# Performance work log

Hardware: AMD Instinct MI355X
Metric: run time of the kernel (lower is better)

Reference implementation:

```python
import jax, jax.numpy as jnp
import numpy as np

NEG_SLOPE = 0.01  # nn.LeakyReLU default


def conv3x3(x, w, b):
    # x: [B,C,H,W], w: [O,I,3,3], stride 1, pad 1
    y = jax.lax.conv_general_dilated(x, w, (1, 1), 'SAME',
                                     dimension_numbers=('NCHW', 'OIHW', 'NCHW'))
    return y + b[None, :, None, None]


def bilinear_gather(img, ys, xs):
    # img: [B,C,H,W]; ys, xs: [B,K,H,W] float sample coords -> [B,C,K,H,W]
    B, C, H, W = img.shape
    imgf = img.reshape(B, C, H * W)
    y0 = jnp.floor(ys)
    x0 = jnp.floor(xs)
    out = jnp.zeros((B, C) + ys.shape[1:], img.dtype)
    for dy in (0, 1):
        for dx in (0, 1):
            yc = y0 + dy
            xc = x0 + dx
            wgt = (1.0 - jnp.abs(ys - yc)) * (1.0 - jnp.abs(xs - xc))
            valid = (yc >= 0) & (yc <= H - 1) & (xc >= 0) & (xc <= W - 1)
            wgt = jnp.where(valid, wgt, 0.0)
            idx = (jnp.clip(yc, 0, H - 1) * W + jnp.clip(xc, 0, W - 1)).astype(jnp.int32)
            g = jax.vmap(lambda f, i: f[:, i])(imgf, idx)  # [B,C,K,H,W]
            out = out + wgt[:, None] * g
    return out


def dcn_v2(x, off_feat, w_off, b_off, w, b):
    # Modulated deformable 3x3 conv (DCNv2Pack, extra_offset_mask=True, dg=1).
    B, C, H, W = x.shape
    om = conv3x3(off_feat, w_off, b_off)            # [B, 27, H, W]
    o1, o2, m = jnp.split(om, 3, axis=1)            # each [B, 9, H, W]
    off = jnp.concatenate([o1, o2], axis=1)         # [B, 18, H, W]
    off_y = off[:, 0::2]                            # [B, 9, H, W]
    off_x = off[:, 1::2]
    mask = jax.nn.sigmoid(m)                        # [B, 9, H, W]
    k = jnp.arange(3, dtype=x.dtype) - 1.0
    ky = jnp.repeat(k, 3)                           # row-major kernel order
    kx = jnp.tile(k, 3)
    hh = jnp.arange(H, dtype=x.dtype)[:, None]
    ww = jnp.arange(W, dtype=x.dtype)[None, :]
    ys = hh[None, None] + ky[None, :, None, None] + off_y
    xs = ww[None, None] + kx[None, :, None, None] + off_x
    sampled = bilinear_gather(x, ys, xs)            # [B,C,9,H,W]
    wk = w.reshape(w.shape[0], C, 9)
    out = jnp.einsum('oik,bkhw,bikhw->bohw', wk, mask, sampled)
    return out + b[None, :, None, None]


def setup_inputs() -> dict:
    key = jax.random.key(0)
    ks = jax.random.split(key, 12)
    B, C, OC, H, W = 4, 64, 32, 128, 128
    s = 0.02
    return {
        'input': jax.random.normal(ks[0], (B, C, H, W), jnp.float32),
        'offset': jax.random.normal(ks[1], (B, OC, H, W), jnp.float32),
        'w_off1': jax.random.normal(ks[2], (27, OC, 3, 3), jnp.float32) * s,
        'b_off1': jnp.zeros((27,), jnp.float32),
        'w1': jax.random.normal(ks[3], (C, C, 3, 3), jnp.float32) * s,
        'b1': jnp.zeros((C,), jnp.float32),
        'w_off2': jax.random.normal(ks[4], (27, OC, 3, 3), jnp.float32) * s,
        'b_off2': jnp.zeros((27,), jnp.float32),
        'w2': jax.random.normal(ks[5], (C, C, 3, 3), jnp.float32) * s,
        'b2': jnp.zeros((C,), jnp.float32),
        'w_last': jax.random.normal(ks[6], (C, C, 3, 3), jnp.float32) * s,
        'b_last': jnp.zeros((C,), jnp.float32),
    }


def reference(input, offset, w_off1, b_off1, w1, b1,
              w_off2, b_off2, w2, b2, w_last, b_last):
    x = dcn_v2(input, offset, w_off1, b_off1, w1, b1)
    x = jnp.where(x >= 0, x, NEG_SLOPE * x)
    out = dcn_v2(x, offset, w_off2, b_off2, w2, b2) + input
    return conv3x3(out, w_last, b_last)
```

## Files before the change

### kernel.cpp

```cpp
#include <hip/hip_runtime.h>
#include <cmath>

#define HW   16384
#define Wd   128
#define Hd   128
#define NB   4

typedef __attribute__((ext_vector_type(8))) _Float16 h16x8;
typedef __attribute__((ext_vector_type(4))) float f32x4;
typedef __attribute__((ext_vector_type(4))) unsigned int u32x4;

__device__ inline unsigned short f2h(float f) {
    _Float16 h = (_Float16)f;
    return __builtin_bit_cast(unsigned short, h);
}
__device__ inline _Float16 u2h(unsigned short u) {
    return __builtin_bit_cast(_Float16, u);
}

__device__ inline void repack_one(int idx, const float* __restrict__ s1, const float* __restrict__ s2,
                                  int Osplit, int O, int CIN, int KS, unsigned short* __restrict__ dst) {
    int e    = idx & 7;
    int lane = (idx >> 3) & 63;
    int ks   = (idx >> 9) % KS;
    int m    = (idx / (512 * KS)) & 3;
    int k    = idx / (2048 * KS);
    int oc = m * 16 + (lane & 15);
    int c  = ks * 32 + (lane >> 4) * 8 + e;
    float v = 0.f;
    if (oc < O && c < CIN)
        v = (oc < Osplit) ? s1[((size_t)oc * CIN + c) * 9 + k]
                          : s2[((size_t)(oc - Osplit) * CIN + c) * 9 + k];
    dst[idx] = f2h(v);
}

__global__ __launch_bounds__(256) void prep(
    const float* __restrict__ input, const float* __restrict__ offset,
    const float* __restrict__ w_off1, const float* __restrict__ w_off2,
    const float* __restrict__ b_off1, const float* __restrict__ b_off2,
    const float* __restrict__ w1, const float* __restrict__ w2, const float* __restrict__ w_last,
    unsigned short* __restrict__ xn, unsigned short* __restrict__ offn,
    unsigned short* __restrict__ wfo, unsigned short* __restrict__ wf1,
    unsigned short* __restrict__ wf2, unsigned short* __restrict__ wfl,
    float* __restrict__ bias54)
{
    int blk = blockIdx.x;
    if (blk < 512) {
        int t = blk * 256 + threadIdx.x;
        if (t < 65536) {
            int b = t >> 14, p = t & 16383;
            const float* s = input + ((size_t)b * 64) * HW + p;
            unsigned short* d = xn + (size_t)t * 64;
#pragma unroll
            for (int g = 0; g < 8; g++) {
                unsigned short pk[8];
#pragma unroll
                for (int e = 0; e < 8; e++) pk[e] = f2h(s[(size_t)(g * 8 + e) * HW]);
                *(u32x4*)(d + g * 8) = *(u32x4*)pk;
            }
        } else {
            int u = t - 65536;
            int b = u >> 14, p = u & 16383;
            const float* s = offset + ((size_t)b * 32) * HW + p;
            unsigned short* d = offn + (size_t)u * 32;
#pragma unroll
            for (int g = 0; g < 4; g++) {
                unsigned short pk[8];
#pragma unroll
                for (int e = 0; e < 8; e++) pk[e] = f2h(s[(size_t)(g * 8 + e) * HW]);
                *(u32x4*)(d + g * 8) = *(u32x4*)pk;
            }
        }
    } else {
        int u = (blk - 512) * 256 + threadIdx.x;
        if (u < 18432)        repack_one(u, w_off1, w_off1, 27, 27, 32, 1, wfo);
        else if (u < 36864)   repack_one(u - 18432, w_off2, w_off2, 27, 27, 32, 1, wfo + 18432);
        else if (u < 73728)   repack_one(u - 36864, w1, w1, 64, 64, 64, 2, wf1);
        else if (u < 110592)  repack_one(u - 73728, w2, w2, 64, 64, 64, 2, wf2);
        else if (u < 147456)  repack_one(u - 110592, w_last, w_last, 64, 64, 64, 2, wfl);
        else if (u < 147510) {
            int j = u - 147456;
            bias54[j] = (j < 27) ? b_off1[j] : b_off2[j - 27];
        }
    }
}

__global__ __launch_bounds__(512, 8) void conv_stage64(
    const unsigned short* __restrict__ xn, const unsigned short* __restrict__ wf,
    const float* __restrict__ bias, float* __restrict__ out)
{
    __shared__ __align__(16) unsigned short stage[198 * 64];
    int lb = ((blockIdx.x & 7) << 7) | (blockIdx.x >> 3);
    int t = threadIdx.x;
    int pxbase = lb * 64;
    int b = pxbase >> 14;
    int pbase = pxbase & 16383;
    int rowbase = pbase >> 7, colbase = pbase & 127;
    const unsigned short* xb = xn + ((size_t)(b << 14)) * 64;

    for (int q = t; q < 1584; q += 512) {
        int ps = q >> 3, j = q & 7;
        int ly = ps / 66, lx = ps - ly * 66;
        int y = rowbase - 1 + ly, x = colbase - 1 + lx;
        bool ok = (y >= 0) & (y < Hd) & (x >= 0) & (x < Wd);
        u32x4 v = {0, 0, 0, 0};
        if (ok) v = *(const u32x4*)(xb + ((size_t)(y * Wd + x)) * 64 + j * 8);
        *(u32x4*)(stage + ps * 64 + ((j ^ (ps & 7)) << 3)) = v;
    }
    __syncthreads();

    int lane = t & 63;
    int wave = t >> 6;
    int kh = wave >> 2;
    int wv = wave & 3;
    int sp = wv * 16 + (lane & 15);
    int px = pxbase + sp;
    int p = px & 16383;
    int cg = lane >> 4;
    int cch = kh * 4 + cg;

    const h16x8* wfv = (const h16x8*)wf;
    f32x4 acc[4];
#pragma unroll
    for (int m = 0; m < 4; m++) acc[m] = (f32x4){0.f, 0.f, 0.f, 0.f};

#pragma unroll
    for (int k = 0; k < 9; k++) {
        int ps = (k / 3) * 66 + sp + (k % 3);
        h16x8 bq = *(const h16x8*)(stage + ps * 64 + ((cch ^ (ps & 7)) << 3));
        h16x8 aF[4];
#pragma unroll
        for (int m = 0; m < 4; m++)
            aF[m] = wfv[((k * 4 + m) * 2 + kh) * 64 + lane];
#pragma unroll
        for (int m = 0; m < 4; m++)
            acc[m] = __builtin_amdgcn_mfma_f32_16x16x32_f16(aF[m], bq, acc[m], 0, 0, 0);
    }

    __syncthreads();
    float* red = (float*)stage;
    if (kh == 1) {
#pragma unroll
        for (int m = 0; m < 4; m++)
#pragma unroll
            for (int j = 0; j < 4; j++)
                red[(m * 4 + j) * 256 + wv * 64 + lane] = acc[m][j];
    }
    __syncthreads();
    if (kh == 0) {
#pragma unroll
        for (int m = 0; m < 4; m++) {
            int ocb = m * 16 + cg * 4;
#pragma unroll
            for (int r = 0; r < 4; r++) {
                int oc = ocb + r;
                float v = acc[m][r] + red[(m * 4 + r) * 256 + wv * 64 + lane] + bias[oc];
                out[((size_t)b * 64 + oc) * HW + p] = v;
            }
        }
    }
}

struct Tap { float w00, w01, w10, w11; int o00, o01, o10, o11; };

__device__ inline Tap mkparams(float oy, float ox, float mv, int row, int col, int k) {
    Tap P;
    float mk = 1.f / (1.f + __expf(-mv));
    float ys = (float)(row + k / 3 - 1) + oy;
    float xs = (float)(col + k % 3 - 1) + ox;
    float y0f = floorf(ys), x0f = floorf(xs);
    float fy = ys - y0f, fx = xs - x0f;
    int y0 = (int)y0f, x0 = (int)x0f;
    int y1 = y0 + 1, x1 = x0 + 1;
    bool vy0 = (y0 >= 0) & (y0 < Hd);
    bool vy1 = (y1 >= 0) & (y1 < Hd);
    bool vx0 = (x0 >= 0) & (x0 < Wd);
    bool vx1 = (x1 >= 0) & (x1 < Wd);
    P.w00 = (vy0 && vx0) ? (1.f - fy) * (1.f - fx) * mk : 0.f;
    P.w01 = (vy0 && vx1) ? (1.f - fy) * fx * mk : 0.f;
    P.w10 = (vy1 && vx0) ? fy * (1.f - fx) * mk : 0.f;
    P.w11 = (vy1 && vx1) ? fy * fx * mk : 0.f;
    int iy0 = min(max(y0, 0), Hd - 1) * Wd;
    int iy1 = min(max(y1, 0), Hd - 1) * Wd;
    int ix0 = min(max(x0, 0), Wd - 1);
    int ix1 = min(max(x1, 0), Wd - 1);
    P.o00 = iy0 + ix0; P.o01 = iy0 + ix1; P.o10 = iy1 + ix0; P.o11 = iy1 + ix1;
    return P;
}

template<int EPI>
__global__ __launch_bounds__(512, 4) void dcn_fused(
    const unsigned short* __restrict__ xn, const unsigned short* __restrict__ offn,
    const unsigned short* __restrict__ wfo, const float* __restrict__ obias,
    const unsigned short* __restrict__ wf, const float* __restrict__ bias,
    const unsigned short* __restrict__ residn, unsigned short* __restrict__ outn)
{
    __shared__ __align__(16) unsigned short stage[490 * 64];
    __shared__ __align__(16) unsigned tbl[576 * 4];

    unsigned short* offstage = stage;
    float* omt = (float*)(stage + 6336);

    int lb = ((blockIdx.x & 7) << 7) | (blockIdx.x >> 3);
    int t = threadIdx.x;
    int pxbase = lb * 64;
    int b = pxbase >> 14;
    int pbase = pxbase & 16383;
    int rowbase = pbase >> 7;
    int colbase = pbase & 127;
    int ybase = rowbase - 3;
    int xbase = colbase - 3;
    const unsigned short* xb = xn + ((size_t)(b << 14)) * 64;
    const unsigned short* ob = offn + ((size_t)(b << 14)) * 32;

    for (int q = t; q < 792; q += 512) {
        int ps = q >> 2, j = q & 3;
        int ly = ps / 66, lx = ps - ly * 66;
        int y = rowbase - 1 + ly, x = colbase - 1 + lx;
        bool ok = (y >= 0) & (y < Hd) & (x >= 0) & (x < Wd);
        u32x4 v = {0, 0, 0, 0};
        if (ok) v = *(const u32x4*)(ob + ((size_t)(y * Wd + x)) * 32 + j * 8);
        *(u32x4*)(offstage + ps * 32 + ((j ^ (ps & 3)) << 3)) = v;
    }
    __syncthreads();

    int lane = t & 63;
    int wave = t >> 6;

    if (wave < 4) {
        int osp = wave * 16 + (lane & 15);
        int cg4 = lane >> 4;
        const h16x8* wfv = (const h16x8*)wfo;
        f32x4 oacc[2];
#pragma unroll
        for (int m = 0; m < 2; m++) oacc[m] = (f32x4){0.f, 0.f, 0.f, 0.f};
#pragma unroll
        for (int k = 0; k < 9; k++) {
            int ps = (k / 3) * 66 + osp + (k % 3);
            h16x8 bq = *(const h16x8*)(offstage + ps * 32 + ((cg4 ^ (ps & 3)) << 3));
#pragma unroll
            for (int m = 0; m < 2; m++) {
                h16x8 aF = wfv[(k * 4 + m) * 64 + lane];
                oacc[m] = __builtin_amdgcn_mfma_f32_16x16x32_f16(aF, bq, oacc[m], 0, 0, 0);
            }
        }
#pragma unroll
        for (int m = 0; m < 2; m++) {
            int ocb = m * 16 + cg4 * 4;
#pragma unroll
            for (int r = 0; r < 4; r++) {
                int oc = ocb + r;
                if (oc < 27) omt[oc * 64 + osp] = oacc[m][r] + obias[oc];
            }
        }
    }
    __syncthreads();

    for (int s = t; s < 576; s += 512) {
        int k = s >> 6, sp2 = s & 63;
        int row = rowbase, col = colbase + sp2;
        float oy = omt[(2 * k) * 64 + sp2];
        float ox = omt[(2 * k + 1) * 64 + sp2];
        float mv = omt[(18 + k) * 64 + sp2];
        Tap P = mkparams(oy, ox, mv, row, col, k);

        unsigned a[4];
        int oo[4] = {P.o00, P.o01, P.o10, P.o11};
#pragma unroll
        for (int c = 0; c < 4; c++) {
            int o = oo[c];
            int y = o >> 7, x = o & 127;
            int ly = y - ybase, lx = x - xbase;
            bool inw = ((unsigned)ly < 7u) & ((unsigned)lx < 70u);
            int ps = min(max(ly, 0), 6) * 70 + min(max(lx, 0), 69);
            a[c] = inw ? (unsigned)((ps << 3) | (ps & 7)) : (0x8000u | (unsigned)o);
        }
        u32x4 pk4 = { a[0] | (a[1] << 16),
                      a[2] | (a[3] << 16),
                      (unsigned)f2h(P.w00) | ((unsigned)f2h(P.w01) << 16),
                      (unsigned)f2h(P.w10) | ((unsigned)f2h(P.w11) << 16) };
        *(u32x4*)&tbl[s * 4] = pk4;
    }
    __syncthreads();

    for (int q = t; q < 3920; q += 512) {
        int ps = q >> 3, j = q & 7;
        int ly = ps / 70, lx = ps - ly * 70;
        int y = min(max(ybase + ly, 0), Hd - 1);
        int x = min(max(xbase + lx, 0), Wd - 1);
        u32x4 v = *(const u32x4*)(xb + ((size_t)(y * Wd + x)) * 64 + j * 8);
        *(u32x4*)(stage + ps * 64 + ((j ^ (ps & 7)) << 3)) = v;
    }
    __syncthreads();

    int kh = wave >> 2;
    int wv = wave & 3;
    int sp = wv * 16 + (lane & 15);
    int px = pxbase + sp;
    int cg = lane >> 4;
    int c0 = kh * 32 + cg * 8;
    int cch = kh * 4 + cg;

    const h16x8* wfv = (const h16x8*)wf;

    f32x4 acc[4];
#pragma unroll
    for (int m = 0; m < 4; m++) acc[m] = (f32x4){0.f, 0.f, 0.f, 0.f};

#pragma unroll
    for (int k = 0; k < 9; k++) {
        int s = k * 64 + sp;
        u32x4 tv = *(const u32x4*)&tbl[s * 4];
        unsigned a01 = tv[0], a23 = tv[1], w01 = tv[2], w23 = tv[3];

        unsigned code[4] = { a01 & 0xffffu, a01 >> 16, a23 & 0xffffu, a23 >> 16 };
        h16x8 gc[4];
#pragma unroll
        for (int c = 0; c < 4; c++)
            gc[c] = *(const h16x8*)((const char*)stage + (((code[c] & 0xFFFu) ^ (unsigned)cch) << 4));

        if (__builtin_expect((a01 | a23) & 0x80008000u, 0)) {
#pragma unroll
            for (int c = 0; c < 4; c++)
                if (code[c] & 0x8000u)
                    gc[c] = *(const h16x8*)(xb + (size_t)(code[c] & 0x7fffu) * 64 + c0);
        }

        _Float16 h00 = u2h((unsigned short)(w01 & 0xffffu));
        _Float16 h01 = u2h((unsigned short)(w01 >> 16));
        _Float16 h10 = u2h((unsigned short)(w23 & 0xffffu));
        _Float16 h11 = u2h((unsigned short)(w23 >> 16));
        h16x8 bF = gc[0] * h00;
        bF = gc[1] * h01 + bF;
        bF = gc[2] * h10 + bF;
        bF = gc[3] * h11 + bF;

        h16x8 aF[4];
#pragma unroll
        for (int m = 0; m < 4; m++)
            aF[m] = wfv[((k * 4 + m) * 2 + kh) * 64 + lane];
#pragma unroll
        for (int m = 0; m < 4; m++)
            acc[m] = __builtin_amdgcn_mfma_f32_16x16x32_f16(aF[m], bF, acc[m], 0, 0, 0);
    }

    __syncthreads();
    float* red = (float*)stage;
    if (kh == 1) {
#pragma unroll
        for (int m = 0; m < 4; m++)
#pragma unroll
            for (int j = 0; j < 4; j++)
                red[(m * 4 + j) * 256 + wv * 64 + lane] = acc[m][j];
    }
    __syncthreads();
    if (kh == 0) {
        unsigned short* drow = outn + (size_t)px * 64;
        const unsigned short* rrow = (EPI == 1) ? residn + (size_t)px * 64 : nullptr;
#pragma unroll
        for (int m = 0; m < 4; m++) {
            int ocb = m * 16 + cg * 4;
            float rv[4] = {0.f, 0.f, 0.f, 0.f};
            if (EPI == 1) {
                ushort4 rr = *(const ushort4*)(rrow + ocb);
                rv[0] = (float)u2h(rr.x); rv[1] = (float)u2h(rr.y);
                rv[2] = (float)u2h(rr.z); rv[3] = (float)u2h(rr.w);
            }
            unsigned short pk[4];
#pragma unroll
            for (int r = 0; r < 4; r++) {
                int oc = ocb + r;
                float v = acc[m][r] + red[(m * 4 + r) * 256 + wv * 64 + lane] + bias[oc];
                if (EPI == 0) v = (v >= 0.f) ? v : 0.01f * v;
                if (EPI == 1) v += rv[r];
                pk[r] = f2h(v);
            }
            *(ushort4*)(drow + ocb) = *(ushort4*)pk;
        }
    }
}

extern "C" void kernel_launch(void* const* d_in, const int* in_sizes, int n_in,
                              void* d_out, int out_size, void* d_ws, size_t ws_size,
                              hipStream_t stream)
{
    const float* input  = (const float*)d_in[0];
    const float* offset = (const float*)d_in[1];
    const float* w_off1 = (const float*)d_in[2];
    const float* b_off1 = (const float*)d_in[3];
    const float* w1     = (const float*)d_in[4];
    const float* b1     = (const float*)d_in[5];
    const float* w_off2 = (const float*)d_in[6];
    const float* b_off2 = (const float*)d_in[7];
    const float* w2     = (const float*)d_in[8];
    const float* b2     = (const float*)d_in[9];
    const float* w_last = (const float*)d_in[10];
    const float* b_last = (const float*)d_in[11];
    float* out = (float*)d_out;

    unsigned short* xn   = (unsigned short*)d_ws;
    unsigned short* offn = xn + 4194304;
    unsigned short* x1n  = offn + 2097152;
    unsigned short* x2n  = x1n + 4194304;
    unsigned short* wfo  = x2n + 4194304;
    unsigned short* wf1  = wfo + 36864;
    unsigned short* wf2  = wf1 + 36864;
    unsigned short* wfl  = wf2 + 36864;
    float* bias54 = (float*)(wfl + 36864);

    prep<<<dim3(1089), 256, 0, stream>>>(input, offset, w_off1, w_off2, b_off1, b_off2,
                                         w1, w2, w_last, xn, offn, wfo, wf1, wf2, wfl, bias54);

    dcn_fused<0><<<dim3(1024), 512, 0, stream>>>(xn, offn, wfo, bias54,
                                                 wf1, b1, nullptr, x1n);
    dcn_fused<1><<<dim3(1024), 512, 0, stream>>>(x1n, offn, wfo + 18432, bias54 + 27,
                                                 wf2, b2, xn, x2n);
    conv_stage64<<<dim3(1024), 512, 0, stream>>>(x2n, wfl, b_last, out);
}
```

Baseline: 80.03 us.

## Slide DCN blocks over two rows reusing a ring-buffered 7-row input stage

Each DCN block now handles two consecutive output rows (half-grid launch) and keeps the input halo in a 7-row circular buffer indexed by y%7. For the second row it loads only the one new row instead of reloading all seven. The offset-conv tile is ring-buffered the same way, and the offset/mask intermediates are stored as fp16 in a shared scratch area that overlaps the table and reduction buffers. This cuts redundant global halo loads, at the cost of half as many blocks, more barriers per block and some lost precision on the offsets.

```diff
diff --git a/kernel.cpp b/kernel.cpp
--- a/kernel.cpp
+++ b/kernel.cpp
@@ -189,194 +189,215 @@
 }
 
 template<int EPI>
-__global__ __launch_bounds__(512, 4) void dcn_fused(
+__global__ __launch_bounds__(512, 4) void dcn_slide(
     const unsigned short* __restrict__ xn, const unsigned short* __restrict__ offn,
     const unsigned short* __restrict__ wfo, const float* __restrict__ obias,
     const unsigned short* __restrict__ wf, const float* __restrict__ bias,
     const unsigned short* __restrict__ residn, unsigned short* __restrict__ outn)
 {
     __shared__ __align__(16) unsigned short stage[490 * 64];
-    __shared__ __align__(16) unsigned tbl[576 * 4];
-
-    unsigned short* offstage = stage;
-    float* omt = (float*)(stage + 6336);
-
-    int lb = ((blockIdx.x & 7) << 7) | (blockIdx.x >> 3);
+    __shared__ __align__(16) char scratch[16512];
+    unsigned short* offstage = (unsigned short*)scratch;
+    unsigned short* omt      = (unsigned short*)(scratch + 12672);
+    unsigned*       tbl      = (unsigned*)scratch;
+    float*          red      = (float*)scratch;
+
+    int Bw = ((blockIdx.x & 7) << 6) | (blockIdx.x >> 3);
     int t = threadIdx.x;
-    int pxbase = lb * 64;
-    int b = pxbase >> 14;
-    int pbase = pxbase & 16383;
-    int rowbase = pbase >> 7;
-    int colbase = pbase & 127;
-    int ybase = rowbase - 3;
-    int xbase = colbase - 3;
-    const unsigned short* xb = xn + ((size_t)(b << 14)) * 64;
-    const unsigned short* ob = offn + ((size_t)(b << 14)) * 32;
-
-    for (int q = t; q < 792; q += 512) {
-        int ps = q >> 2, j = q & 3;
-        int ly = ps / 66, lx = ps - ly * 66;
-        int y = rowbase - 1 + ly, x = colbase - 1 + lx;
-        bool ok = (y >= 0) & (y < Hd) & (x >= 0) & (x < Wd);
-        u32x4 v = {0, 0, 0, 0};
-        if (ok) v = *(const u32x4*)(ob + ((size_t)(y * Wd + x)) * 32 + j * 8);
-        *(u32x4*)(offstage + ps * 32 + ((j ^ (ps & 3)) << 3)) = v;
-    }
-    __syncthreads();
-
     int lane = t & 63;
     int wave = t >> 6;
-
-    if (wave < 4) {
-        int osp = wave * 16 + (lane & 15);
-        int cg4 = lane >> 4;
-        const h16x8* wfv = (const h16x8*)wfo;
-        f32x4 oacc[2];
-#pragma unroll
-        for (int m = 0; m < 2; m++) oacc[m] = (f32x4){0.f, 0.f, 0.f, 0.f};
-#pragma unroll
-        for (int k = 0; k < 9; k++) {
-            int ps = (k / 3) * 66 + osp + (k % 3);
-            h16x8 bq = *(const h16x8*)(offstage + ps * 32 + ((cg4 ^ (ps & 3)) << 3));
-#pragma unroll
-            for (int m = 0; m < 2; m++) {
-                h16x8 aF = wfv[(k * 4 + m) * 64 + lane];
-                oacc[m] = __builtin_amdgcn_mfma_f32_16x16x32_f16(aF, bq, oacc[m], 0, 0, 0);
-            }
-        }
-#pragma unroll
-        for (int m = 0; m < 2; m++) {
-            int ocb = m * 16 + cg4 * 4;
-#pragma unroll
-            for (int r = 0; r < 4; r++) {
-                int oc = ocb + r;
-                if (oc < 27) omt[oc * 64 + osp] = oacc[m][r] + obias[oc];
-            }
-        }
-    }
-    __syncthreads();
-
-    for (int s = t; s < 576; s += 512) {
-        int k = s >> 6, sp2 = s & 63;
-        int row = rowbase, col = colbase + sp2;
-        float oy = omt[(2 * k) * 64 + sp2];
-        float ox = omt[(2 * k + 1) * 64 + sp2];
-        float mv = omt[(18 + k) * 64 + sp2];
-        Tap P = mkparams(oy, ox, mv, row, col, k);
-
-        unsigned a[4];
-        int oo[4] = {P.o00, P.o01, P.o10, P.o11};
-#pragma unroll
-        for (int c = 0; c < 4; c++) {
-            int o = oo[c];
-            int y = o >> 7, x = o & 127;
-            int ly = y - ybase, lx = x - xbase;
-            bool inw = ((unsigned)ly < 7u) & ((unsigned)lx < 70u);
-            int ps = min(max(ly, 0), 6) * 70 + min(max(lx, 0), 69);
-            a[c] = inw ? (unsigned)((ps << 3) | (ps & 7)) : (0x8000u | (unsigned)o);
-        }
-        u32x4 pk4 = { a[0] | (a[1] << 16),
-                      a[2] | (a[3] << 16),
-                      (unsigned)f2h(P.w00) | ((unsigned)f2h(P.w01) << 16),
-                      (unsigned)f2h(P.w10) | ((unsigned)f2h(P.w11) << 16) };
-        *(u32x4*)&tbl[s * 4] = pk4;
-    }
-    __syncthreads();
-
-    for (int q = t; q < 3920; q += 512) {
-        int ps = q >> 3, j = q & 7;
-        int ly = ps / 70, lx = ps - ly * 70;
-        int y = min(max(ybase + ly, 0), Hd - 1);
-        int x = min(max(xbase + lx, 0), Wd - 1);
-        u32x4 v = *(const u32x4*)(xb + ((size_t)(y * Wd + x)) * 64 + j * 8);
-        *(u32x4*)(stage + ps * 64 + ((j ^ (ps & 7)) << 3)) = v;
-    }
-    __syncthreads();
-
     int kh = wave >> 2;
     int wv = wave & 3;
-    int sp = wv * 16 + (lane & 15);
-    int px = pxbase + sp;
     int cg = lane >> 4;
     int c0 = kh * 32 + cg * 8;
     int cch = kh * 4 + cg;
-
+    int sp = wv * 16 + (lane & 15);
+
+    int b  = Bw >> 7;
+    int rp = (Bw >> 1) & 63;
+    int ch = Bw & 1;
+    int r0 = rp * 2;
+    int colbase = ch * 64;
+    int xbase = colbase - 3;
+
+    const unsigned short* xb = xn + ((size_t)(b << 14)) * 64;
+    const unsigned short* ob = offn + ((size_t)(b << 14)) * 32;
     const h16x8* wfv = (const h16x8*)wf;
-
-    f32x4 acc[4];
-#pragma unroll
-    for (int m = 0; m < 4; m++) acc[m] = (f32x4){0.f, 0.f, 0.f, 0.f};
-
-#pragma unroll
-    for (int k = 0; k < 9; k++) {
-        int s = k * 64 + sp;
-        u32x4 tv = *(const u32x4*)&tbl[s * 4];
-        unsigned a01 = tv[0], a23 = tv[1], w01 = tv[2], w23 = tv[3];
-
-        unsigned code[4] = { a01 & 0xffffu, a01 >> 16, a23 & 0xffffu, a23 >> 16 };
-        h16x8 gc[4];
-#pragma unroll
-        for (int c = 0; c < 4; c++)
-            gc[c] = *(const h16x8*)((const char*)stage + (((code[c] & 0xFFFu) ^ (unsigned)cch) << 4));
-
-        if (__builtin_expect((a01 | a23) & 0x80008000u, 0)) {
+    const h16x8* wfvo = (const h16x8*)wfo;
+
+    for (int si = 0; si < 2; ++si) {
+        int rowbase = r0 + si;
+        int ybase = rowbase - 3;
+        int pbase = (rowbase << 7) + colbase;
+
+        for (int q = t; q < 792; q += 512) {
+            int psl = q >> 2, j = q & 3;
+            int ly = psl / 66, lx = psl - ly * 66;
+            int wy = rowbase - 1 + ly;
+            int x = colbase - 1 + lx;
+            int slab = (wy + 129) % 3;
+            int ps = slab * 66 + lx;
+            bool ok = (wy >= 0) & (wy < Hd) & (x >= 0) & (x < Wd);
+            u32x4 v = {0, 0, 0, 0};
+            if (ok) v = *(const u32x4*)(ob + ((size_t)(wy * Wd + x)) * 32 + j * 8);
+            *(u32x4*)(offstage + ps * 32 + ((j ^ (ps & 3)) << 3)) = v;
+        }
+        if (si == 0) {
+            for (int q = t; q < 3920; q += 512) {
+                int psl = q >> 3, j = q & 7;
+                int ly = psl / 70, lx = psl - ly * 70;
+                int y = min(max(ybase + ly, 0), Hd - 1);
+                int x = min(max(xbase + lx, 0), Wd - 1);
+                int ps = (y % 7) * 70 + lx;
+                u32x4 v = *(const u32x4*)(xb + ((size_t)(y * Wd + x)) * 64 + j * 8);
+                *(u32x4*)(stage + ps * 64 + ((j ^ (ps & 7)) << 3)) = v;
+            }
+        } else {
+            for (int q = t; q < 560; q += 512) {
+                int lx = q >> 3, j = q & 7;
+                int y = min(rowbase + 3, Hd - 1);
+                int x = min(max(xbase + lx, 0), Wd - 1);
+                int ps = (y % 7) * 70 + lx;
+                u32x4 v = *(const u32x4*)(xb + ((size_t)(y * Wd + x)) * 64 + j * 8);
+                *(u32x4*)(stage + ps * 64 + ((j ^ (ps & 7)) << 3)) = v;
+            }
+        }
+        __syncthreads();
+
+        if (wave < 4) {
+            int osp = wave * 16 + (lane & 15);
+            int cg4 = lane >> 4;
+            f32x4 oacc[2];
+#pragma unroll
+            for (int m = 0; m < 2; m++) oacc[m] = (f32x4){0.f, 0.f, 0.f, 0.f};
+#pragma unroll
+            for (int k = 0; k < 9; k++) {
+                int wy = rowbase - 1 + k / 3;
+                int slab = (wy + 129) % 3;
+                int ps = slab * 66 + osp + (k % 3);
+                h16x8 bq = *(const h16x8*)(offstage + ps * 32 + ((cg4 ^ (ps & 3)) << 3));
+#pragma unroll
+                for (int m = 0; m < 2; m++) {
+                    h16x8 aF = wfvo[(k * 4 + m) * 64 + lane];
+                    oacc[m] = __builtin_amdgcn_mfma_f32_16x16x32_f16(aF, bq, oacc[m], 0, 0, 0);
+                }
+            }
+#pragma unroll
+            for (int m = 0; m < 2; m++) {
+                int ocb = m * 16 + cg4 * 4;
+#pragma unroll
+                for (int r = 0; r < 4; r++) {
+                    int oc = ocb + r;
+                    if (oc < 27) omt[oc * 64 + osp] = f2h(oacc[m][r] + obias[oc]);
+                }
+            }
+        }
+        __syncthreads();
+
+        for (int s = t; s < 576; s += 512) {
+            int k = s >> 6, sp2 = s & 63;
+            int row = rowbase, col = colbase + sp2;
+            float oy = (float)u2h(omt[(2 * k) * 64 + sp2]);
+            float ox = (float)u2h(omt[(2 * k + 1) * 64 + sp2]);
+            float mv = (float)u2h(omt[(18 + k) * 64 + sp2]);
+            Tap P = mkparams(oy, ox, mv, row, col, k);
+
+            unsigned a[4];
+            int oo[4] = {P.o00, P.o01, P.o10, P.o11};
+#pragma unroll
+            for (int c = 0; c < 4; c++) {
+                int o = oo[c];
+                int y = o >> 7, x = o & 127;
+                int ly = y - ybase, lx = x - xbase;
+                bool inw = ((unsigned)ly < 7u) & ((unsigned)lx < 70u);
+                int ps = (y % 7) * 70 + min(max(lx, 0), 69);
+                a[c] = inw ? (unsigned)((ps << 3) | (ps & 7)) : (0x8000u | (unsigned)o);
+            }
+            u32x4 pk4 = { a[0] | (a[1] << 16),
+                          a[2] | (a[3] << 16),
+                          (unsigned)f2h(P.w00) | ((unsigned)f2h(P.w01) << 16),
+                          (unsigned)f2h(P.w10) | ((unsigned)f2h(P.w11) << 16) };
+            *(u32x4*)&tbl[s * 4] = pk4;
+        }
+        __syncthreads();
+
+        f32x4 acc[4];
+#pragma unroll
+        for (int m = 0; m < 4; m++) acc[m] = (f32x4){0.f, 0.f, 0.f, 0.f};
+
+#pragma unroll
+        for (int k = 0; k < 9; k++) {
+            int s = k * 64 + sp;
+            u32x4 tv = *(const u32x4*)&tbl[s * 4];
+            unsigned a01 = tv[0], a23 = tv[1], w01 = tv[2], w23 = tv[3];
+
+            unsigned code[4] = { a01 & 0xffffu, a01 >> 16, a23 & 0xffffu, a23 >> 16 };
+            h16x8 gc[4];
 #pragma unroll
             for (int c = 0; c < 4; c++)
-                if (code[c] & 0x8000u)
-                    gc[c] = *(const h16x8*)(xb + (size_t)(code[c] & 0x7fffu) * 64 + c0);
-        }
-
-        _Float16 h00 = u2h((unsigned short)(w01 & 0xffffu));
-        _Float16 h01 = u2h((unsigned short)(w01 >> 16));
-        _Float16 h10 = u2h((unsigned short)(w23 & 0xffffu));
-        _Float16 h11 = u2h((unsigned short)(w23 >> 16));
-        h16x8 bF = gc[0] * h00;
-        bF = gc[1] * h01 + bF;
-        bF = gc[2] * h10 + bF;
-        bF = gc[3] * h11 + bF;
-
-        h16x8 aF[4];
-#pragma unroll
-        for (int m = 0; m < 4; m++)
-            aF[m] = wfv[((k * 4 + m) * 2 + kh) * 64 + lane];
-#pragma unroll
-        for (int m = 0; m < 4; m++)
-            acc[m] = __builtin_amdgcn_mfma_f32_16x16x32_f16(aF[m], bF, acc[m], 0, 0, 0);
-    }
-
-    __syncthreads();
-    float* red = (float*)stage;
-    if (kh == 1) {
-#pragma unroll
-        for (int m = 0; m < 4; m++)
-#pragma unroll
-            for (int j = 0; j < 4; j++)
-                red[(m * 4 + j) * 256 + wv * 64 + lane] = acc[m][j];
-    }
-    __syncthreads();
-    if (kh == 0) {
-        unsigned short* drow = outn + (size_t)px * 64;
-        const unsigned short* rrow = (EPI == 1) ? residn + (size_t)px * 64 : nullptr;
-#pragma unroll
-        for (int m = 0; m < 4; m++) {
-            int ocb = m * 16 + cg * 4;
-            float rv[4] = {0.f, 0.f, 0.f, 0.f};
-            if (EPI == 1) {
-                ushort4 rr = *(const ushort4*)(rrow + ocb);
-                rv[0] = (float)u2h(rr.x); rv[1] = (float)u2h(rr.y);
-                rv[2] = (float)u2h(rr.z); rv[3] = (float)u2h(rr.w);
-            }
-            unsigned short pk[4];
-#pragma unroll
-            for (int r = 0; r < 4; r++) {
-                int oc = ocb + r;
-                float v = acc[m][r] + red[(m * 4 + r) * 256 + wv * 64 + lane] + bias[oc];
-                if (EPI == 0) v = (v >= 0.f) ? v : 0.01f * v;
-                if (EPI == 1) v += rv[r];
-                pk[r] = f2h(v);
-            }
-            *(ushort4*)(drow + ocb) = *(ushort4*)pk;
-        }
+                gc[c] = *(const h16x8*)((const char*)stage + (((code[c] & 0xFFFu) ^ (unsigned)cch) << 4));
+
+            if (__builtin_expect((a01 | a23) & 0x80008000u, 0)) {
+#pragma unroll
+                for (int c = 0; c < 4; c++)
+                    if (code[c] & 0x8000u)
+                        gc[c] = *(const h16x8*)(xb + (size_t)(code[c] & 0x7fffu) * 64 + c0);
+            }
+
+            _Float16 h00 = u2h((unsigned short)(w01 & 0xffffu));
+            _Float16 h01 = u2h((unsigned short)(w01 >> 16));
+            _Float16 h10 = u2h((unsigned short)(w23 & 0xffffu));
+            _Float16 h11 = u2h((unsigned short)(w23 >> 16));
+            h16x8 bF = gc[0] * h00;
+            bF = gc[1] * h01 + bF;
+            bF = gc[2] * h10 + bF;
+            bF = gc[3] * h11 + bF;
+
+            h16x8 aF[4];
+#pragma unroll
+            for (int m = 0; m < 4; m++)
+                aF[m] = wfv[((k * 4 + m) * 2 + kh) * 64 + lane];
+#pragma unroll
+            for (int m = 0; m < 4; m++)
+                acc[m] = __builtin_amdgcn_mfma_f32_16x16x32_f16(aF[m], bF, acc[m], 0, 0, 0);
+        }
+        __syncthreads();
+
+        if (kh == 1) {
+#pragma unroll
+            for (int m = 0; m < 4; m++)
+#pragma unroll
+                for (int j = 0; j < 4; j++)
+                    red[(m * 4 + j) * 256 + wv * 64 + lane] = acc[m][j];
+        }
+        __syncthreads();
+
+        if (kh == 0) {
+            int px = (b << 14) + pbase + sp;
+            unsigned short* drow = outn + (size_t)px * 64;
+            const unsigned short* rrow = (EPI == 1) ? residn + (size_t)px * 64 : nullptr;
+#pragma unroll
+            for (int m = 0; m < 4; m++) {
+                int ocb = m * 16 + cg * 4;
+                float rv[4] = {0.f, 0.f, 0.f, 0.f};
+                if (EPI == 1) {
+                    ushort4 rr = *(const ushort4*)(rrow + ocb);
+                    rv[0] = (float)u2h(rr.x); rv[1] = (float)u2h(rr.y);
+                    rv[2] = (float)u2h(rr.z); rv[3] = (float)u2h(rr.w);
+                }
+                unsigned short pk[4];
+#pragma unroll
+                for (int r = 0; r < 4; r++) {
+                    int oc = ocb + r;
+                    float v = acc[m][r] + red[(m * 4 + r) * 256 + wv * 64 + lane] + bias[oc];
+                    if (EPI == 0) v = (v >= 0.f) ? v : 0.01f * v;
+                    if (EPI == 1) v += rv[r];
+                    pk[r] = f2h(v);
+                }
+                *(ushort4*)(drow + ocb) = *(ushort4*)pk;
+            }
+        }
+        __syncthreads();
     }
 }
 
@@ -411,9 +432,9 @@
     prep<<<dim3(1089), 256, 0, stream>>>(input, offset, w_off1, w_off2, b_off1, b_off2,
                                          w1, w2, w_last, xn, offn, wfo, wf1, wf2, wfl, bias54);
 
-    dcn_fused<0><<<dim3(1024), 512, 0, stream>>>(xn, offn, wfo, bias54,
-                                                 wf1, b1, nullptr, x1n);
-    dcn_fused<1><<<dim3(1024), 512, 0, stream>>>(x1n, offn, wfo + 18432, bias54 + 27,
-                                                 wf2, b2, xn, x2n);
+    dcn_slide<0><<<dim3(512), 512, 0, stream>>>(xn, offn, wfo, bias54,
+                                                wf1, b1, nullptr, x1n);
+    dcn_slide<1><<<dim3(512), 512, 0, stream>>>(x1n, offn, wfo + 18432, bias54 + 27,
+                                                wf2, b2, xn, x2n);
     conv_stage64<<<dim3(1024), 512, 0, stream>>>(x2n, wfl, b_last, out);
 }
```

New measurement: 172.4 us. 2.15x slower.
